# Performance work log

Measured on AMD Instinct MI355X. Metric: run time of the kernel, lower is better.

Reference implementation:

```python
import jax, jax.numpy as jnp
import numpy as np

N_NODES = 50000
N_EDGES = 800000
IN_C, HID_C, OUT_C = 128, 128, 64


def setup_inputs() -> dict:
    key = jax.random.key(0)
    ks = jax.random.split(key, 12)
    glorot = lambda k, shape: jax.random.normal(k, shape, dtype=jnp.float32) * (2.0 / (shape[0] + shape[-1])) ** 0.5
    return {
        "x": jax.random.normal(ks[0], (N_NODES, IN_C), dtype=jnp.float32),
        "edge_index": jax.random.randint(ks[1], (2, N_EDGES), 0, N_NODES, dtype=jnp.int64),
        "W_s1": glorot(ks[2], (IN_C, HID_C)), "b_s1": jnp.zeros((HID_C,), jnp.float32),
        "W_s2": glorot(ks[3], (HID_C, HID_C)), "b_s2": jnp.zeros((HID_C,), jnp.float32),
        "W_m1": glorot(ks[4], (IN_C, HID_C)), "b_m1": jnp.zeros((HID_C,), jnp.float32),
        "W_m21": glorot(ks[5], (IN_C, HID_C)), "b_m21": jnp.zeros((HID_C,), jnp.float32),
        "W_m22": glorot(ks[6], (HID_C, HID_C)), "b_m22": jnp.zeros((HID_C,), jnp.float32),
        "W_att": glorot(ks[7], (HID_C, 1)), "b_att": jnp.zeros((1,), jnp.float32),
        "W_fc": glorot(ks[8], (2 * HID_C, OUT_C)), "b_fc": jnp.zeros((OUT_C,), jnp.float32),
    }


def _gcn_conv(x, W, b, src, dst, n_nodes):
    """PyG GCNConv: add self-loops, symmetric deg^-1/2 norm, linear, scatter-add, bias."""
    xw = x @ W  # [N, H]
    loop = jnp.arange(n_nodes, dtype=src.dtype)
    s = jnp.concatenate([src, loop])
    d = jnp.concatenate([dst, loop])
    ones = jnp.ones(s.shape[0], dtype=x.dtype)
    deg = jax.ops.segment_sum(ones, d, num_segments=n_nodes)  # in-degree incl. self loop
    dinv = jnp.where(deg > 0, jax.lax.rsqrt(deg), 0.0)
    norm = dinv[s] * dinv[d]  # [E+N]
    msg = xw[s] * norm[:, None]
    return jax.ops.segment_sum(msg, d, num_segments=n_nodes) + b


def reference(x, edge_index, W_s1, b_s1, W_s2, b_s2, W_m1, b_m1, W_m21, b_m21,
              W_m22, b_m22, W_att, b_att, W_fc, b_fc):
    n = x.shape[0]
    src, dst = edge_index[0], edge_index[1]
    # structural branch: two GCN layers
    h_struct = jax.nn.relu(_gcn_conv(x, W_s1, b_s1, src, dst, n))
    h_struct = jax.nn.relu(_gcn_conv(h_struct, W_s2, b_s2, src, dst, n))
    # meta branches
    h1 = jax.nn.relu(_gcn_conv(x, W_m1, b_m1, src, dst, n))
    h2 = jax.nn.relu(_gcn_conv(x, W_m21, b_m21, src, dst, n))
    h2 = jax.nn.relu(_gcn_conv(h2, W_m22, b_m22, src, dst, n))
    # attention-weighted fusion over the 2 branches
    H = jnp.stack([h1, h2], axis=1)  # [N, 2, H]
    attn_scores = H @ W_att + b_att  # [N, 2, 1]
    attn_weights = jax.nn.softmax(attn_scores, axis=1)
    h_meta = jnp.sum(attn_weights * H, axis=1)  # [N, H]
    h_comb = jnp.concatenate([h_struct, h_meta], axis=1)  # [N, 2H]
    return h_comb @ W_fc + b_fc  # [N, OUT_C]
```

## Files before the change

kernel.cpp:

```cpp
#include <hip/hip_runtime.h>
#include <hip/hip_bf16.h>

#define N_NODES 50000
#define N_EDGES 800000

#define SCAN_BS 256
#define SCAN_NB ((N_NODES + SCAN_BS - 1) / SCAN_BS)

#define PREP_CVT_NB   6250
#define PREP_DEG_NB   3125
#define PREP_WCAT_NB  192
#define PREP_TP_NB    64
#define PREP_NB (PREP_CVT_NB + PREP_DEG_NB + PREP_WCAT_NB + 3 * PREP_TP_NB)

typedef __attribute__((ext_vector_type(8))) short bf16x8;
typedef __attribute__((ext_vector_type(4))) float f32x4;

__device__ __forceinline__ ushort f2bf(float f) {
    unsigned u = __float_as_uint(f);
    return (ushort)((u + 0x7fffu + ((u >> 16) & 1u)) >> 16);
}
__device__ __forceinline__ float bf2f(ushort u) {
    return __uint_as_float(((unsigned)u) << 16);
}

__global__ __launch_bounds__(256)
void prep_kernel(const float* __restrict__ x, uint2* __restrict__ xb4,
                 const int* __restrict__ edst, int* __restrict__ hist,
                 const float* __restrict__ Ws1, const float* __restrict__ Wm21,
                 const float* __restrict__ Wm1,
                 const float* __restrict__ bs1, const float* __restrict__ bm21,
                 const float* __restrict__ bm1,
                 ushort* __restrict__ Wcat_t, float* __restrict__ bcat,
                 const float* __restrict__ Ws2, ushort* __restrict__ Ws2t,
                 const float* __restrict__ Wm22, ushort* __restrict__ Wm22t,
                 const float* __restrict__ Wfc, ushort* __restrict__ Wfct,
                 int* __restrict__ row_ptr) {
    const int bid = blockIdx.x;
    const int t = threadIdx.x;
    if (bid < PREP_CVT_NB) {
        int i = bid * 256 + t;
        float4 v = *(const float4*)&x[(size_t)i * 4];
        uint2 o;
        o.x = (uint)f2bf(v.x) | ((uint)f2bf(v.y) << 16);
        o.y = (uint)f2bf(v.z) | ((uint)f2bf(v.w) << 16);
        xb4[i] = o;
    } else if (bid < PREP_CVT_NB + PREP_DEG_NB) {
        int e = (bid - PREP_CVT_NB) * 256 + t;
        atomicAdd(&hist[edst[e]], 1);
    } else if (bid < PREP_CVT_NB + PREP_DEG_NB + PREP_WCAT_NB) {
        int idx = (bid - PREP_CVT_NB - PREP_DEG_NB) * 256 + t;
        int c = idx >> 7, k = idx & 127;
        float v = (c < 128) ? Ws1[k * 128 + c]
                : (c < 256) ? Wm21[k * 128 + (c - 128)]
                            : Wm1[k * 128 + (c - 256)];
        Wcat_t[idx] = f2bf(v);
        if (idx < 384) {
            bcat[idx] = (idx < 128) ? bs1[idx] : (idx < 256) ? bm21[idx - 128] : bm1[idx - 256];
        }
        if (idx == 0) row_ptr[N_NODES] = N_EDGES;
    } else if (bid < PREP_CVT_NB + PREP_DEG_NB + PREP_WCAT_NB + PREP_TP_NB) {
        int idx = (bid - PREP_CVT_NB - PREP_DEG_NB - PREP_WCAT_NB) * 256 + t;
        int c = idx >> 7, k = idx & 127;
        Ws2t[idx] = f2bf(Ws2[(size_t)k * 128 + c]);
    } else if (bid < PREP_CVT_NB + PREP_DEG_NB + PREP_WCAT_NB + 2 * PREP_TP_NB) {
        int idx = (bid - PREP_CVT_NB - PREP_DEG_NB - PREP_WCAT_NB - PREP_TP_NB) * 256 + t;
        int c = idx >> 7, k = idx & 127;
        Wm22t[idx] = f2bf(Wm22[(size_t)k * 128 + c]);
    } else {
        int idx = (bid - PREP_CVT_NB - PREP_DEG_NB - PREP_WCAT_NB - 2 * PREP_TP_NB) * 256 + t;
        int c = idx >> 8, k = idx & 255;
        Wfct[idx] = f2bf(Wfc[(size_t)k * 64 + c]);
    }
}

__global__ __launch_bounds__(SCAN_BS)
void scan1_kernel(const int* __restrict__ hist, int* __restrict__ bsum,
                  float* __restrict__ dinv, int n) {
    __shared__ int s[SCAN_BS];
    int t = threadIdx.x;
    int i = blockIdx.x * SCAN_BS + t;
    int v = (i < n) ? hist[i] : 0;
    if (i < n) dinv[i] = rsqrtf((float)(v + 1));
    s[t] = v;
    __syncthreads();
#pragma unroll
    for (int off = SCAN_BS / 2; off > 0; off >>= 1) {
        if (t < off) s[t] += s[t + off];
        __syncthreads();
    }
    if (t == 0) bsum[blockIdx.x] = s[0];
}

__global__ __launch_bounds__(SCAN_BS)
void scan3_kernel(const int* __restrict__ hist, const int* __restrict__ bsum,
                  int* __restrict__ row_ptr, int* __restrict__ cursor, int n) {
    __shared__ int s[SCAN_BS];
    __shared__ int pre_s;
    int t = threadIdx.x;
    int b = blockIdx.x;
    int p = 0;
    for (int j = t; j < b; j += SCAN_BS) p += bsum[j];
    s[t] = p;
    __syncthreads();
#pragma unroll
    for (int off = SCAN_BS / 2; off > 0; off >>= 1) {
        if (t < off) s[t] += s[t + off];
        __syncthreads();
    }
    if (t == 0) pre_s = s[0];
    __syncthreads();
    const int pre = pre_s;
    __syncthreads();
    int i = b * SCAN_BS + t;
    int v = (i < n) ? hist[i] : 0;
    s[t] = v;
    __syncthreads();
#pragma unroll
    for (int off = 1; off < SCAN_BS; off <<= 1) {
        int tmp = (t >= off) ? s[t - off] : 0;
        __syncthreads();
        s[t] += tmp;
        __syncthreads();
    }
    if (i < n) {
        int ex = s[t] - v + pre;
        row_ptr[i] = ex;
        cursor[i]  = ex;
    }
}

__global__ void fill_kernel(const int* __restrict__ src, const int* __restrict__ dst, int E,
                            int* __restrict__ cursor, int2* __restrict__ edge_data,
                            const float* __restrict__ dinv) {
    int e = blockIdx.x * blockDim.x + threadIdx.x;
    if (e < E) {
        int d = dst[e];
        int s = src[e];
        int pos = atomicAdd(&cursor[d], 1);
        edge_data[pos] = make_int2(s, __float_as_int(dinv[s]));
    }
}

template<int C>
__global__ __launch_bounds__(256)
void agg_bf16(const ushort* __restrict__ X, int ldx,
              ushort* __restrict__ Y, int ldy,
              const int* __restrict__ row_ptr,
              const int2* __restrict__ edge_data,
              const float* __restrict__ dinv, int n) {
    constexpr int CG = C / 8;
    constexpr int SLOTS = 64 / CG;
    const int wid = blockIdx.x * (blockDim.x >> 6) + (threadIdx.x >> 6);
    if (wid >= n) return;
    const int lane = threadIdx.x & 63;
    const int cg = lane & (CG - 1);
    const int slot = lane / CG;

    const float di = dinv[wid];
    float acc[8] = {0.f, 0.f, 0.f, 0.f, 0.f, 0.f, 0.f, 0.f};

    auto fma_row = [&](uint4 v, float w) {
        acc[0] = fmaf(w, __uint_as_float(v.x << 16), acc[0]);
        acc[1] = fmaf(w, __uint_as_float(v.x & 0xffff0000u), acc[1]);
        acc[2] = fmaf(w, __uint_as_float(v.y << 16), acc[2]);
        acc[3] = fmaf(w, __uint_as_float(v.y & 0xffff0000u), acc[3]);
        acc[4] = fmaf(w, __uint_as_float(v.z << 16), acc[4]);
        acc[5] = fmaf(w, __uint_as_float(v.z & 0xffff0000u), acc[5]);
        acc[6] = fmaf(w, __uint_as_float(v.w << 16), acc[6]);
        acc[7] = fmaf(w, __uint_as_float(v.w & 0xffff0000u), acc[7]);
    };

    if (slot == 0) {
        uint4 v = *(const uint4*)&X[(size_t)wid * ldx + cg * 8];
        fma_row(v, di * di);
    }
    const int e0 = row_ptr[wid], e1 = row_ptr[wid + 1];
    int e = e0 + slot;
    for (; e + 3 * SLOTS < e1; e += 4 * SLOTS) {
        const int2 d0 = edge_data[e];
        const int2 d1 = edge_data[e + SLOTS];
        const int2 d2 = edge_data[e + 2 * SLOTS];
        const int2 d3 = edge_data[e + 3 * SLOTS];
        const uint4 v0 = *(const uint4*)&X[(size_t)d0.x * ldx + cg * 8];
        const uint4 v1 = *(const uint4*)&X[(size_t)d1.x * ldx + cg * 8];
        const uint4 v2 = *(const uint4*)&X[(size_t)d2.x * ldx + cg * 8];
        const uint4 v3 = *(const uint4*)&X[(size_t)d3.x * ldx + cg * 8];
        fma_row(v0, di * __int_as_float(d0.y));
        fma_row(v1, di * __int_as_float(d1.y));
        fma_row(v2, di * __int_as_float(d2.y));
        fma_row(v3, di * __int_as_float(d3.y));
    }
    for (; e < e1; e += SLOTS) {
        const int2 d0 = edge_data[e];
        const uint4 v0 = *(const uint4*)&X[(size_t)d0.x * ldx + cg * 8];
        fma_row(v0, di * __int_as_float(d0.y));
    }
#pragma unroll
    for (int j = 0; j < 8; ++j) {
        if (SLOTS == 4) acc[j] += __shfl_xor(acc[j], 16);
        if (SLOTS >= 2) acc[j] += __shfl_xor(acc[j], 32);
    }
    if (slot == 0) {
        uint4 o;
        o.x = (uint)f2bf(acc[0]) | ((uint)f2bf(acc[1]) << 16);
        o.y = (uint)f2bf(acc[2]) | ((uint)f2bf(acc[3]) << 16);
        o.z = (uint)f2bf(acc[4]) | ((uint)f2bf(acc[5]) << 16);
        o.w = (uint)f2bf(acc[6]) | ((uint)f2bf(acc[7]) << 16);
        *(uint4*)&Y[(size_t)wid * ldy + cg * 8] = o;
    }
}

__global__ __launch_bounds__(256)
void mfma_gemm_kernel(const ushort* __restrict__ A, int lda,
                      const ushort* __restrict__ Wt,
                      const float* __restrict__ bias,
                      ushort* __restrict__ Y, int ldy, int M) {
    __shared__ char Asmem[128 * 272];
    const int tid = threadIdx.x;
    const int lane = tid & 63;
    const int w = tid >> 6;
    const int rb = blockIdx.x * 128;
    const int cb = blockIdx.y * 128;

    {
        const int rowbase = tid >> 4;
        const int seg = tid & 15;
#pragma unroll
        for (int it = 0; it < 8; ++it) {
            int row = it * 16 + rowbase;
            uint4 v = make_uint4(0u, 0u, 0u, 0u);
            int r = rb + row;
            if (r < M) v = *(const uint4*)&A[(size_t)r * lda + seg * 8];
            *(uint4*)&Asmem[row * 272 + seg * 16] = v;
        }
    }
    __syncthreads();

    f32x4 acc[2][8];
#pragma unroll
    for (int i = 0; i < 2; ++i)
#pragma unroll
        for (int j = 0; j < 8; ++j) acc[i][j] = (f32x4){0.f, 0.f, 0.f, 0.f};

    const int arow0 = w * 32 + (lane & 15);
    const int kq = (lane >> 4) * 8;
    const int ccol = lane & 15;
#pragma unroll
    for (int ks = 0; ks < 4; ++ks) {
        const int k0 = ks * 32;
        const bf16x8 a0 = *(const bf16x8*)&Asmem[arow0 * 272 + (k0 + kq) * 2];
        const bf16x8 a1 = *(const bf16x8*)&Asmem[(arow0 + 16) * 272 + (k0 + kq) * 2];
#pragma unroll
        for (int ct = 0; ct < 8; ++ct) {
            const bf16x8 b = *(const bf16x8*)&Wt[(size_t)(cb + ct * 16 + ccol) * 128 + k0 + kq];
            acc[0][ct] = __builtin_amdgcn_mfma_f32_16x16x32_bf16(a0, b, acc[0][ct], 0, 0, 0);
            acc[1][ct] = __builtin_amdgcn_mfma_f32_16x16x32_bf16(a1, b, acc[1][ct], 0, 0, 0);
        }
    }

    const int rowq = (lane >> 4) * 4;
#pragma unroll
    for (int rt = 0; rt < 2; ++rt) {
#pragma unroll
        for (int ct = 0; ct < 8; ++ct) {
            const int col = cb + ct * 16 + ccol;
            const float bcol = bias[col];
#pragma unroll
            for (int r = 0; r < 4; ++r) {
                const int row = rb + w * 32 + rt * 16 + rowq + r;
                if (row >= M) continue;
                Y[(size_t)row * ldy + col] = f2bf(fmaxf(acc[rt][ct][r] + bcol, 0.f));
            }
        }
    }
}

__global__ __launch_bounds__(512, 4)
void gemm2fc_kernel(const ushort* __restrict__ bufB,
                    const ushort* __restrict__ Ws2t, const float* __restrict__ bs2,
                    const ushort* __restrict__ Wm22t, const float* __restrict__ bm22,
                    const ushort* __restrict__ cat1,
                    const float* __restrict__ Watt, const float* __restrict__ batt,
                    const ushort* __restrict__ Wfct, const float* __restrict__ bfc,
                    float* __restrict__ Y, int M) {
    __shared__ __align__(16) char smem[69632];
    const int tid = threadIdx.x;
    const int rb = blockIdx.x * 128;

    {
        const int seg = tid & 15;
        const int rowbase = tid >> 4;
#pragma unroll
        for (int it = 0; it < 8; ++it) {
            int idx = it * 32 + rowbase;
            int region = idx >> 7;
            int row = idx & 127;
            int r = rb + row;
            uint4 v = make_uint4(0u, 0u, 0u, 0u);
            if (r < M) v = *(const uint4*)&bufB[(size_t)r * 256 + region * 128 + seg * 8];
            *(uint4*)&smem[region * 34816 + row * 272 + seg * 16] = v;
        }
    }
    __syncthreads();

    const int w = tid >> 6;
    const int lane = tid & 63;
    const int branch = w >> 2;
    const int wl = w & 3;
    const char* Areg = smem + branch * 34816;
    const ushort* Wt = branch ? Wm22t : Ws2t;
    const float* bias = branch ? bm22 : bs2;

    f32x4 acc[2][8];
#pragma unroll
    for (int i = 0; i < 2; ++i)
#pragma unroll
        for (int j = 0; j < 8; ++j) acc[i][j] = (f32x4){0.f, 0.f, 0.f, 0.f};

    const int arow0 = wl * 32 + (lane & 15);
    const int kq = (lane >> 4) * 8;
    const int ccol = lane & 15;
#pragma unroll
    for (int ks = 0; ks < 4; ++ks) {
        const int k0 = ks * 32;
        const bf16x8 a0 = *(const bf16x8*)&Areg[arow0 * 272 + (k0 + kq) * 2];
        const bf16x8 a1 = *(const bf16x8*)&Areg[(arow0 + 16) * 272 + (k0 + kq) * 2];
#pragma unroll
        for (int ct = 0; ct < 8; ++ct) {
            const bf16x8 b = *(const bf16x8*)&Wt[(size_t)(ct * 16 + ccol) * 128 + k0 + kq];
            acc[0][ct] = __builtin_amdgcn_mfma_f32_16x16x32_bf16(a0, b, acc[0][ct], 0, 0, 0);
            acc[1][ct] = __builtin_amdgcn_mfma_f32_16x16x32_bf16(a1, b, acc[1][ct], 0, 0, 0);
        }
    }

#pragma unroll
    for (int rt = 0; rt < 2; ++rt)
#pragma unroll
        for (int ct = 0; ct < 8; ++ct) {
            const float bcol = bias[ct * 16 + ccol];
#pragma unroll
            for (int r = 0; r < 4; ++r)
                acc[rt][ct][r] = fmaxf(acc[rt][ct][r] + bcol, 0.f);
        }

    const int quad = lane >> 4;
    if (branch == 1) {
        float wv[8];
#pragma unroll
        for (int ct = 0; ct < 8; ++ct) wv[ct] = Watt[ct * 16 + ccol];
        const float ba = batt[0];
#pragma unroll
        for (int rt = 0; rt < 2; ++rt) {
#pragma unroll
            for (int r = 0; r < 4; ++r) {
                const int row0 = rb + wl * 32 + rt * 16 + quad * 4 + r;
                const int rowc = (row0 < M) ? row0 : (M - 1);
                const ushort* h1row = &cat1[(size_t)rowc * 384 + 256];
                float bp = 0.f, ap = 0.f;
#pragma unroll
                for (int ct = 0; ct < 8; ++ct) {
                    bp += acc[rt][ct][r] * wv[ct];
                    ap += bf2f(h1row[ct * 16 + ccol]) * wv[ct];
                }
#pragma unroll
                for (int off = 1; off < 16; off <<= 1) {
                    bp += __shfl_xor(bp, off);
                    ap += __shfl_xor(ap, off);
                }
                const float a = ap + ba, b = bp + ba;
                const float m = fmaxf(a, b);
                const float ea = __expf(a - m), eb = __expf(b - m);
                const float inv = 1.f / (ea + eb);
                const float wa = ea * inv, wb = eb * inv;
#pragma unroll
                for (int ct = 0; ct < 8; ++ct) {
                    const float h1 = bf2f(h1row[ct * 16 + ccol]);
                    acc[rt][ct][r] = fmaf(wa, h1, wb * acc[rt][ct][r]);
                }
            }
        }
    }
    __syncthreads();

#pragma unroll
    for (int rt = 0; rt < 2; ++rt) {
#pragma unroll
        for (int ct = 0; ct < 8; ++ct) {
            const int col = branch * 128 + ct * 16 + ccol;
#pragma unroll
            for (int r = 0; r < 4; ++r) {
                const int row = wl * 32 + rt * 16 + quad * 4 + r;
                *(ushort*)&smem[row * 528 + col * 2] = f2bf(acc[rt][ct][r]);
            }
        }
    }
    __syncthreads();

    f32x4 fcacc[4];
#pragma unroll
    for (int j = 0; j < 4; ++j) fcacc[j] = (f32x4){0.f, 0.f, 0.f, 0.f};
    const int frow = w * 16 + (lane & 15);
#pragma unroll
    for (int ks = 0; ks < 8; ++ks) {
        const int k0 = ks * 32;
        const bf16x8 a = *(const bf16x8*)&smem[frow * 528 + (k0 + kq) * 2];
#pragma unroll
        for (int ct = 0; ct < 4; ++ct) {
            const bf16x8 b = *(const bf16x8*)&Wfct[(size_t)(ct * 16 + ccol) * 256 + k0 + kq];
            fcacc[ct] = __builtin_amdgcn_mfma_f32_16x16x32_bf16(a, b, fcacc[ct], 0, 0, 0);
        }
    }
#pragma unroll
    for (int ct = 0; ct < 4; ++ct) {
        const int col = ct * 16 + ccol;
        const float bcol = bfc[col];
#pragma unroll
        for (int r = 0; r < 4; ++r) {
            const int row = rb + w * 16 + quad * 4 + r;
            if (row < M) Y[(size_t)row * 64 + col] = fcacc[ct][r] + bcol;
        }
    }
}

extern "C" void kernel_launch(void* const* d_in, const int* in_sizes, int n_in,
                              void* d_out, int out_size, void* d_ws, size_t ws_size,
                              hipStream_t stream) {
    const int N = N_NODES, E = N_EDGES;
    const float* x     = (const float*)d_in[0];
    const int*   ei    = (const int*)d_in[1];
    const int*   esrc  = ei;
    const int*   edst  = ei + E;
    const float* W_s1  = (const float*)d_in[2];
    const float* b_s1  = (const float*)d_in[3];
    const float* W_s2  = (const float*)d_in[4];
    const float* b_s2  = (const float*)d_in[5];
    const float* W_m1  = (const float*)d_in[6];
    const float* b_m1  = (const float*)d_in[7];
    const float* W_m21 = (const float*)d_in[8];
    const float* b_m21 = (const float*)d_in[9];
    const float* W_m22 = (const float*)d_in[10];
    const float* b_m22 = (const float*)d_in[11];
    const float* W_att = (const float*)d_in[12];
    const float* b_att = (const float*)d_in[13];
    const float* W_fc  = (const float*)d_in[14];
    const float* b_fc  = (const float*)d_in[15];
    float* out = (float*)d_out;

    char* base = (char*)d_ws;
    size_t off = 0;
    auto take = [&](size_t nbytes) -> void* {
        void* p = base + off;
        off += (nbytes + 255) & ~(size_t)255;
        return p;
    };
    int*    hist      = (int*)take((size_t)N * 4);
    int*    cursor    = (int*)take((size_t)N * 4);
    int*    row_ptr   = (int*)take((size_t)(N + 1) * 4);
    int*    bsum      = (int*)take((size_t)SCAN_NB * 4);
    int2*   edge_data = (int2*)take((size_t)E * 8);
    float*  dinv      = (float*)take((size_t)N * 4);
    ushort* xb        = (ushort*)take((size_t)N * 128 * 2);
    ushort* agg_x     = (ushort*)take((size_t)N * 128 * 2);
    ushort* cat1      = (ushort*)take((size_t)N * 384 * 2);
    ushort* bufB      = (ushort*)take((size_t)N * 256 * 2);
    ushort* Wcat_t    = (ushort*)take((size_t)384 * 128 * 2);
    ushort* Ws2_t     = (ushort*)take((size_t)128 * 128 * 2);
    ushort* Wm22_t    = (ushort*)take((size_t)128 * 128 * 2);
    ushort* Wfc_t     = (ushort*)take((size_t)64 * 256 * 2);
    float*  bcat      = (float*)take((size_t)384 * 4);

    hipMemsetAsync(hist, 0, (size_t)N * 4, stream);
    prep_kernel<<<PREP_NB, 256, 0, stream>>>(x, (uint2*)xb, edst, hist,
                                             W_s1, W_m21, W_m1, b_s1, b_m21, b_m1,
                                             Wcat_t, bcat, W_s2, Ws2_t, W_m22, Wm22_t,
                                             W_fc, Wfc_t, row_ptr);
    scan1_kernel<<<SCAN_NB, SCAN_BS, 0, stream>>>(hist, bsum, dinv, N);
    scan3_kernel<<<SCAN_NB, SCAN_BS, 0, stream>>>(hist, bsum, row_ptr, cursor, N);
    fill_kernel<<<(E + 255) / 256, 256, 0, stream>>>(esrc, edst, E, cursor, edge_data, dinv);

    agg_bf16<128><<<(N + 3) / 4, 256, 0, stream>>>(xb, 128, agg_x, 128, row_ptr, edge_data, dinv, N);
    dim3 gm384((N + 127) / 128, 3);
    mfma_gemm_kernel<<<gm384, 256, 0, stream>>>(agg_x, 128, Wcat_t, bcat, cat1, 384, N);
    agg_bf16<256><<<(N + 3) / 4, 256, 0, stream>>>(cat1, 384, bufB, 256, row_ptr, edge_data, dinv, N);
    gemm2fc_kernel<<<(N + 127) / 128, 512, 0, stream>>>(bufB, Ws2_t, b_s2, Wm22_t, b_m22,
                                                        cat1, W_att, b_att, Wfc_t, b_fc, out, N);
}
```

Measured before the change: 375.7 us.

## Slice feature matrices into 32-channel planes for cache-friendly gather aggregation

Node features are stored as separate 32-column slices, each contiguous across nodes, and the aggregation kernel gives each block one slice. The goal is a smaller gather working set per slice, so repeated neighbor rows stay in L2/MALL and fewer 64-byte lines are fetched per edge. In exchange, edge lists and row pointers are re-read once per slice, and the GEMM epilogue now writes scattered slice-layout output with per-column branching. The h1 branch is split into its own buffer.

```diff
diff --git a/kernel.cpp b/kernel.cpp
--- a/kernel.cpp
+++ b/kernel.cpp
@@ -25,7 +25,7 @@
 }
 
 __global__ __launch_bounds__(256)
-void prep_kernel(const float* __restrict__ x, uint2* __restrict__ xb4,
+void prep_kernel(const float* __restrict__ x, uint2* __restrict__ xbs4,
                  const int* __restrict__ edst, int* __restrict__ hist,
                  const float* __restrict__ Ws1, const float* __restrict__ Wm21,
                  const float* __restrict__ Wm1,
@@ -44,7 +44,11 @@
         uint2 o;
         o.x = (uint)f2bf(v.x) | ((uint)f2bf(v.y) << 16);
         o.y = (uint)f2bf(v.z) | ((uint)f2bf(v.w) << 16);
-        xb4[i] = o;
+        int node = i >> 5;
+        int g = i & 31;
+        int slice = g >> 3;
+        int wi = g & 7;
+        xbs4[((size_t)slice * N_NODES + node) * 8 + wi] = o;
     } else if (bid < PREP_CVT_NB + PREP_DEG_NB) {
         int e = (bid - PREP_CVT_NB) * 256 + t;
         atomicAdd(&hist[edst[e]], 1);
@@ -142,72 +146,73 @@
     }
 }
 
-template<int C>
+template<int NSLICES>
 __global__ __launch_bounds__(256)
-void agg_bf16(const ushort* __restrict__ X, int ldx,
-              ushort* __restrict__ Y, int ldy,
-              const int* __restrict__ row_ptr,
-              const int2* __restrict__ edge_data,
-              const float* __restrict__ dinv, int n) {
-    constexpr int CG = C / 8;
-    constexpr int SLOTS = 64 / CG;
-    const int wid = blockIdx.x * (blockDim.x >> 6) + (threadIdx.x >> 6);
-    if (wid >= n) return;
-    const int lane = threadIdx.x & 63;
-    const int cg = lane & (CG - 1);
-    const int slot = lane / CG;
-
-    const float di = dinv[wid];
-    float acc[8] = {0.f, 0.f, 0.f, 0.f, 0.f, 0.f, 0.f, 0.f};
-
-    auto fma_row = [&](uint4 v, float w) {
-        acc[0] = fmaf(w, __uint_as_float(v.x << 16), acc[0]);
-        acc[1] = fmaf(w, __uint_as_float(v.x & 0xffff0000u), acc[1]);
-        acc[2] = fmaf(w, __uint_as_float(v.y << 16), acc[2]);
-        acc[3] = fmaf(w, __uint_as_float(v.y & 0xffff0000u), acc[3]);
-        acc[4] = fmaf(w, __uint_as_float(v.z << 16), acc[4]);
-        acc[5] = fmaf(w, __uint_as_float(v.z & 0xffff0000u), acc[5]);
-        acc[6] = fmaf(w, __uint_as_float(v.w << 16), acc[6]);
-        acc[7] = fmaf(w, __uint_as_float(v.w & 0xffff0000u), acc[7]);
-    };
-
-    if (slot == 0) {
-        uint4 v = *(const uint4*)&X[(size_t)wid * ldx + cg * 8];
-        fma_row(v, di * di);
-    }
-    const int e0 = row_ptr[wid], e1 = row_ptr[wid + 1];
-    int e = e0 + slot;
-    for (; e + 3 * SLOTS < e1; e += 4 * SLOTS) {
-        const int2 d0 = edge_data[e];
-        const int2 d1 = edge_data[e + SLOTS];
-        const int2 d2 = edge_data[e + 2 * SLOTS];
-        const int2 d3 = edge_data[e + 3 * SLOTS];
-        const uint4 v0 = *(const uint4*)&X[(size_t)d0.x * ldx + cg * 8];
-        const uint4 v1 = *(const uint4*)&X[(size_t)d1.x * ldx + cg * 8];
-        const uint4 v2 = *(const uint4*)&X[(size_t)d2.x * ldx + cg * 8];
-        const uint4 v3 = *(const uint4*)&X[(size_t)d3.x * ldx + cg * 8];
-        fma_row(v0, di * __int_as_float(d0.y));
-        fma_row(v1, di * __int_as_float(d1.y));
-        fma_row(v2, di * __int_as_float(d2.y));
-        fma_row(v3, di * __int_as_float(d3.y));
-    }
-    for (; e < e1; e += SLOTS) {
-        const int2 d0 = edge_data[e];
-        const uint4 v0 = *(const uint4*)&X[(size_t)d0.x * ldx + cg * 8];
-        fma_row(v0, di * __int_as_float(d0.y));
-    }
-#pragma unroll
-    for (int j = 0; j < 8; ++j) {
-        if (SLOTS == 4) acc[j] += __shfl_xor(acc[j], 16);
-        if (SLOTS >= 2) acc[j] += __shfl_xor(acc[j], 32);
-    }
-    if (slot == 0) {
-        uint4 o;
-        o.x = (uint)f2bf(acc[0]) | ((uint)f2bf(acc[1]) << 16);
-        o.y = (uint)f2bf(acc[2]) | ((uint)f2bf(acc[3]) << 16);
-        o.z = (uint)f2bf(acc[4]) | ((uint)f2bf(acc[5]) << 16);
-        o.w = (uint)f2bf(acc[6]) | ((uint)f2bf(acc[7]) << 16);
-        *(uint4*)&Y[(size_t)wid * ldy + cg * 8] = o;
+void agg_sliced(const ushort* __restrict__ Xs,
+                ushort* __restrict__ Y, int ldy,
+                const int* __restrict__ row_ptr,
+                const int2* __restrict__ edge_data,
+                const float* __restrict__ dinv, int n) {
+    const int slice = blockIdx.x % NSLICES;
+    const int grp   = blockIdx.x / NSLICES;
+    const int wave  = threadIdx.x >> 6;
+    const int lane  = threadIdx.x & 63;
+    const int chunk = lane & 3;
+    const int slot  = lane >> 2;
+    const ushort* X = Xs + (size_t)slice * n * 32;
+
+#pragma unroll 1
+    for (int nd = 0; nd < 4; ++nd) {
+        const int node = grp * 16 + wave * 4 + nd;
+        if (node >= n) break;
+        const float di = dinv[node];
+        float acc[8] = {0.f, 0.f, 0.f, 0.f, 0.f, 0.f, 0.f, 0.f};
+
+        auto fma_row = [&](uint4 v, float w) {
+            acc[0] = fmaf(w, __uint_as_float(v.x << 16), acc[0]);
+            acc[1] = fmaf(w, __uint_as_float(v.x & 0xffff0000u), acc[1]);
+            acc[2] = fmaf(w, __uint_as_float(v.y << 16), acc[2]);
+            acc[3] = fmaf(w, __uint_as_float(v.y & 0xffff0000u), acc[3]);
+            acc[4] = fmaf(w, __uint_as_float(v.z << 16), acc[4]);
+            acc[5] = fmaf(w, __uint_as_float(v.z & 0xffff0000u), acc[5]);
+            acc[6] = fmaf(w, __uint_as_float(v.w << 16), acc[6]);
+            acc[7] = fmaf(w, __uint_as_float(v.w & 0xffff0000u), acc[7]);
+        };
+
+        if (slot == 0) {
+            uint4 v = *(const uint4*)&X[(size_t)node * 32 + chunk * 8];
+            fma_row(v, di * di);
+        }
+        const int e0 = row_ptr[node], e1 = row_ptr[node + 1];
+        int e = e0 + slot;
+        for (; e + 16 < e1; e += 32) {
+            const int2 d0 = edge_data[e];
+            const int2 d1 = edge_data[e + 16];
+            const uint4 v0 = *(const uint4*)&X[(size_t)d0.x * 32 + chunk * 8];
+            const uint4 v1 = *(const uint4*)&X[(size_t)d1.x * 32 + chunk * 8];
+            fma_row(v0, di * __int_as_float(d0.y));
+            fma_row(v1, di * __int_as_float(d1.y));
+        }
+        if (e < e1) {
+            const int2 d0 = edge_data[e];
+            const uint4 v0 = *(const uint4*)&X[(size_t)d0.x * 32 + chunk * 8];
+            fma_row(v0, di * __int_as_float(d0.y));
+        }
+#pragma unroll
+        for (int j = 0; j < 8; ++j) {
+            acc[j] += __shfl_xor(acc[j], 4);
+            acc[j] += __shfl_xor(acc[j], 8);
+            acc[j] += __shfl_xor(acc[j], 16);
+            acc[j] += __shfl_xor(acc[j], 32);
+        }
+        if (slot == 0) {
+            uint4 o;
+            o.x = (uint)f2bf(acc[0]) | ((uint)f2bf(acc[1]) << 16);
+            o.y = (uint)f2bf(acc[2]) | ((uint)f2bf(acc[3]) << 16);
+            o.z = (uint)f2bf(acc[4]) | ((uint)f2bf(acc[5]) << 16);
+            o.w = (uint)f2bf(acc[6]) | ((uint)f2bf(acc[7]) << 16);
+            *(uint4*)&Y[(size_t)node * ldy + slice * 32 + chunk * 8] = o;
+        }
     }
 }
 
@@ -215,7 +220,7 @@
 void mfma_gemm_kernel(const ushort* __restrict__ A, int lda,
                       const ushort* __restrict__ Wt,
                       const float* __restrict__ bias,
-                      ushort* __restrict__ Y, int ldy, int M) {
+                      ushort* __restrict__ catA, ushort* __restrict__ h1, int M) {
     __shared__ char Asmem[128 * 272];
     const int tid = threadIdx.x;
     const int lane = tid & 63;
@@ -265,12 +270,16 @@
 #pragma unroll
         for (int ct = 0; ct < 8; ++ct) {
             const int col = cb + ct * 16 + ccol;
-            const float bcol = bias[col];
 #pragma unroll
             for (int r = 0; r < 4; ++r) {
                 const int row = rb + w * 32 + rt * 16 + rowq + r;
                 if (row >= M) continue;
-                Y[(size_t)row * ldy + col] = f2bf(fmaxf(acc[rt][ct][r] + bcol, 0.f));
+                float v = fmaxf(acc[rt][ct][r] + bias[col], 0.f);
+                ushort bv = f2bf(v);
+                if (col < 256)
+                    catA[((size_t)(col >> 5) * N_NODES + row) * 32 + (col & 31)] = bv;
+                else
+                    h1[(size_t)row * 128 + (col - 256)] = bv;
             }
         }
     }
@@ -280,7 +289,7 @@
 void gemm2fc_kernel(const ushort* __restrict__ bufB,
                     const ushort* __restrict__ Ws2t, const float* __restrict__ bs2,
                     const ushort* __restrict__ Wm22t, const float* __restrict__ bm22,
-                    const ushort* __restrict__ cat1,
+                    const ushort* __restrict__ h1buf,
                     const float* __restrict__ Watt, const float* __restrict__ batt,
                     const ushort* __restrict__ Wfct, const float* __restrict__ bfc,
                     float* __restrict__ Y, int M) {
@@ -356,7 +365,7 @@
             for (int r = 0; r < 4; ++r) {
                 const int row0 = rb + wl * 32 + rt * 16 + quad * 4 + r;
                 const int rowc = (row0 < M) ? row0 : (M - 1);
-                const ushort* h1row = &cat1[(size_t)rowc * 384 + 256];
+                const ushort* h1row = &h1buf[(size_t)rowc * 128];
                 float bp = 0.f, ap = 0.f;
 #pragma unroll
                 for (int ct = 0; ct < 8; ++ct) {
@@ -460,9 +469,10 @@
     int*    bsum      = (int*)take((size_t)SCAN_NB * 4);
     int2*   edge_data = (int2*)take((size_t)E * 8);
     float*  dinv      = (float*)take((size_t)N * 4);
-    ushort* xb        = (ushort*)take((size_t)N * 128 * 2);
+    ushort* xbs       = (ushort*)take((size_t)N * 128 * 2);
     ushort* agg_x     = (ushort*)take((size_t)N * 128 * 2);
-    ushort* cat1      = (ushort*)take((size_t)N * 384 * 2);
+    ushort* catA      = (ushort*)take((size_t)N * 256 * 2);
+    ushort* h1buf     = (ushort*)take((size_t)N * 128 * 2);
     ushort* bufB      = (ushort*)take((size_t)N * 256 * 2);
     ushort* Wcat_t    = (ushort*)take((size_t)384 * 128 * 2);
     ushort* Ws2_t     = (ushort*)take((size_t)128 * 128 * 2);
@@ -471,7 +481,7 @@
     float*  bcat      = (float*)take((size_t)384 * 4);
 
     hipMemsetAsync(hist, 0, (size_t)N * 4, stream);
-    prep_kernel<<<PREP_NB, 256, 0, stream>>>(x, (uint2*)xb, edst, hist,
+    prep_kernel<<<PREP_NB, 256, 0, stream>>>(x, (uint2*)xbs, edst, hist,
                                              W_s1, W_m21, W_m1, b_s1, b_m21, b_m1,
                                              Wcat_t, bcat, W_s2, Ws2_t, W_m22, Wm22_t,
                                              W_fc, Wfc_t, row_ptr);
@@ -479,10 +489,11 @@
     scan3_kernel<<<SCAN_NB, SCAN_BS, 0, stream>>>(hist, bsum, row_ptr, cursor, N);
     fill_kernel<<<(E + 255) / 256, 256, 0, stream>>>(esrc, edst, E, cursor, edge_data, dinv);
 
-    agg_bf16<128><<<(N + 3) / 4, 256, 0, stream>>>(xb, 128, agg_x, 128, row_ptr, edge_data, dinv, N);
+    const int NGRP = (N + 15) / 16;
+    agg_sliced<4><<<NGRP * 4, 256, 0, stream>>>(xbs, agg_x, 128, row_ptr, edge_data, dinv, N);
     dim3 gm384((N + 127) / 128, 3);
-    mfma_gemm_kernel<<<gm384, 256, 0, stream>>>(agg_x, 128, Wcat_t, bcat, cat1, 384, N);
-    agg_bf16<256><<<(N + 3) / 4, 256, 0, stream>>>(cat1, 384, bufB, 256, row_ptr, edge_data, dinv, N);
+    mfma_gemm_kernel<<<gm384, 256, 0, stream>>>(agg_x, 128, Wcat_t, bcat, catA, h1buf, N);
+    agg_sliced<8><<<NGRP * 8, 256, 0, stream>>>(catA, bufB, 256, row_ptr, edge_data, dinv, N);
     gemm2fc_kernel<<<(N + 127) / 128, 512, 0, stream>>>(bufB, Ws2_t, b_s2, Wm22_t, b_m22,
-                                                        cat1, W_att, b_att, Wfc_t, b_fc, out, N);
-}
+                                                        h1buf, W_att, b_att, Wfc_t, b_fc, out, N);
+}
```

New measurement: 496.1 us. 1.32x slower.

## Fuse first-layer neighbor aggregation into the 384-wide MFMA GEMM kernel

Applied to the files above, without the earlier changes.

Merges the bf16 aggregation of x and the first-layer GEMM into one kernel. Each wave aggregates 16 nodes into shared memory, then runs MFMA against all 384 output columns. This removes the agg_x intermediate's global write and re-read plus one launch. In exchange each wave processes its 16 nodes one after another (4 edge slots per node instead of wave-per-node), the block count drops, and each wave holds 24 accumulator tiles, so occupancy and latency hiding may suffer.

```diff
diff --git a/kernel.cpp b/kernel.cpp
--- a/kernel.cpp
+++ b/kernel.cpp
@@ -212,66 +212,107 @@
 }
 
 __global__ __launch_bounds__(256)
-void mfma_gemm_kernel(const ushort* __restrict__ A, int lda,
+void agg_gemm1_kernel(const ushort* __restrict__ xb,
+                      const int* __restrict__ row_ptr,
+                      const int2* __restrict__ edge_data,
+                      const float* __restrict__ dinv,
                       const ushort* __restrict__ Wt,
                       const float* __restrict__ bias,
-                      ushort* __restrict__ Y, int ldy, int M) {
-    __shared__ char Asmem[128 * 272];
+                      ushort* __restrict__ cat1, int n) {
+    __shared__ __align__(16) char smem[64 * 272];
     const int tid = threadIdx.x;
+    const int w = tid >> 6;
     const int lane = tid & 63;
-    const int w = tid >> 6;
-    const int rb = blockIdx.x * 128;
-    const int cb = blockIdx.y * 128;
-
-    {
-        const int rowbase = tid >> 4;
-        const int seg = tid & 15;
-#pragma unroll
-        for (int it = 0; it < 8; ++it) {
-            int row = it * 16 + rowbase;
-            uint4 v = make_uint4(0u, 0u, 0u, 0u);
-            int r = rb + row;
-            if (r < M) v = *(const uint4*)&A[(size_t)r * lda + seg * 8];
-            *(uint4*)&Asmem[row * 272 + seg * 16] = v;
-        }
-    }
-    __syncthreads();
-
-    f32x4 acc[2][8];
-#pragma unroll
-    for (int i = 0; i < 2; ++i)
-#pragma unroll
-        for (int j = 0; j < 8; ++j) acc[i][j] = (f32x4){0.f, 0.f, 0.f, 0.f};
-
-    const int arow0 = w * 32 + (lane & 15);
+    const int rb = blockIdx.x * 64;
+    const int row0 = w * 16;
+    char* myrows = smem + row0 * 272;
+
+    const int cg = lane & 15;
+    const int slot = lane >> 4;
+#pragma unroll 1
+    for (int nd = 0; nd < 16; ++nd) {
+        const int node = rb + row0 + nd;
+        float acc[8] = {0.f, 0.f, 0.f, 0.f, 0.f, 0.f, 0.f, 0.f};
+        auto fma_row = [&](uint4 v, float wgt) {
+            acc[0] = fmaf(wgt, __uint_as_float(v.x << 16), acc[0]);
+            acc[1] = fmaf(wgt, __uint_as_float(v.x & 0xffff0000u), acc[1]);
+            acc[2] = fmaf(wgt, __uint_as_float(v.y << 16), acc[2]);
+            acc[3] = fmaf(wgt, __uint_as_float(v.y & 0xffff0000u), acc[3]);
+            acc[4] = fmaf(wgt, __uint_as_float(v.z << 16), acc[4]);
+            acc[5] = fmaf(wgt, __uint_as_float(v.z & 0xffff0000u), acc[5]);
+            acc[6] = fmaf(wgt, __uint_as_float(v.w << 16), acc[6]);
+            acc[7] = fmaf(wgt, __uint_as_float(v.w & 0xffff0000u), acc[7]);
+        };
+        if (node < n) {
+            const float di = dinv[node];
+            if (slot == 0) {
+                uint4 v = *(const uint4*)&xb[(size_t)node * 128 + cg * 8];
+                fma_row(v, di * di);
+            }
+            const int e0 = row_ptr[node], e1 = row_ptr[node + 1];
+            int e = e0 + slot;
+            for (; e + 12 < e1; e += 16) {
+                const int2 d0 = edge_data[e];
+                const int2 d1 = edge_data[e + 4];
+                const int2 d2 = edge_data[e + 8];
+                const int2 d3 = edge_data[e + 12];
+                const uint4 v0 = *(const uint4*)&xb[(size_t)d0.x * 128 + cg * 8];
+                const uint4 v1 = *(const uint4*)&xb[(size_t)d1.x * 128 + cg * 8];
+                const uint4 v2 = *(const uint4*)&xb[(size_t)d2.x * 128 + cg * 8];
+                const uint4 v3 = *(const uint4*)&xb[(size_t)d3.x * 128 + cg * 8];
+                fma_row(v0, di * __int_as_float(d0.y));
+                fma_row(v1, di * __int_as_float(d1.y));
+                fma_row(v2, di * __int_as_float(d2.y));
+                fma_row(v3, di * __int_as_float(d3.y));
+            }
+            for (; e < e1; e += 4) {
+                const int2 d0 = edge_data[e];
+                const uint4 v0 = *(const uint4*)&xb[(size_t)d0.x * 128 + cg * 8];
+                fma_row(v0, di * __int_as_float(d0.y));
+            }
+        }
+#pragma unroll
+        for (int j = 0; j < 8; ++j) {
+            acc[j] += __shfl_xor(acc[j], 16);
+            acc[j] += __shfl_xor(acc[j], 32);
+        }
+        if (slot == 0) {
+            uint4 o;
+            o.x = (uint)f2bf(acc[0]) | ((uint)f2bf(acc[1]) << 16);
+            o.y = (uint)f2bf(acc[2]) | ((uint)f2bf(acc[3]) << 16);
+            o.z = (uint)f2bf(acc[4]) | ((uint)f2bf(acc[5]) << 16);
+            o.w = (uint)f2bf(acc[6]) | ((uint)f2bf(acc[7]) << 16);
+            *(uint4*)&myrows[nd * 272 + cg * 16] = o;
+        }
+    }
+
+    f32x4 acc2[24];
+#pragma unroll
+    for (int j = 0; j < 24; ++j) acc2[j] = (f32x4){0.f, 0.f, 0.f, 0.f};
+    const int arow = lane & 15;
     const int kq = (lane >> 4) * 8;
     const int ccol = lane & 15;
 #pragma unroll
     for (int ks = 0; ks < 4; ++ks) {
         const int k0 = ks * 32;
-        const bf16x8 a0 = *(const bf16x8*)&Asmem[arow0 * 272 + (k0 + kq) * 2];
-        const bf16x8 a1 = *(const bf16x8*)&Asmem[(arow0 + 16) * 272 + (k0 + kq) * 2];
-#pragma unroll
-        for (int ct = 0; ct < 8; ++ct) {
-            const bf16x8 b = *(const bf16x8*)&Wt[(size_t)(cb + ct * 16 + ccol) * 128 + k0 + kq];
-            acc[0][ct] = __builtin_amdgcn_mfma_f32_16x16x32_bf16(a0, b, acc[0][ct], 0, 0, 0);
-            acc[1][ct] = __builtin_amdgcn_mfma_f32_16x16x32_bf16(a1, b, acc[1][ct], 0, 0, 0);
+        const bf16x8 a = *(const bf16x8*)&myrows[arow * 272 + (k0 + kq) * 2];
+#pragma unroll
+        for (int ct = 0; ct < 24; ++ct) {
+            const bf16x8 b = *(const bf16x8*)&Wt[(size_t)(ct * 16 + ccol) * 128 + k0 + kq];
+            acc2[ct] = __builtin_amdgcn_mfma_f32_16x16x32_bf16(a, b, acc2[ct], 0, 0, 0);
         }
     }
 
     const int rowq = (lane >> 4) * 4;
 #pragma unroll
-    for (int rt = 0; rt < 2; ++rt) {
-#pragma unroll
-        for (int ct = 0; ct < 8; ++ct) {
-            const int col = cb + ct * 16 + ccol;
-            const float bcol = bias[col];
-#pragma unroll
-            for (int r = 0; r < 4; ++r) {
-                const int row = rb + w * 32 + rt * 16 + rowq + r;
-                if (row >= M) continue;
-                Y[(size_t)row * ldy + col] = f2bf(fmaxf(acc[rt][ct][r] + bcol, 0.f));
-            }
+    for (int ct = 0; ct < 24; ++ct) {
+        const int col = ct * 16 + ccol;
+        const float bcol = bias[col];
+#pragma unroll
+        for (int r = 0; r < 4; ++r) {
+            const int row = rb + row0 + rowq + r;
+            if (row < n)
+                cat1[(size_t)row * 384 + col] = f2bf(fmaxf(acc2[ct][r] + bcol, 0.f));
         }
     }
 }
@@ -461,7 +502,6 @@
     int2*   edge_data = (int2*)take((size_t)E * 8);
     float*  dinv      = (float*)take((size_t)N * 4);
     ushort* xb        = (ushort*)take((size_t)N * 128 * 2);
-    ushort* agg_x     = (ushort*)take((size_t)N * 128 * 2);
     ushort* cat1      = (ushort*)take((size_t)N * 384 * 2);
     ushort* bufB      = (ushort*)take((size_t)N * 256 * 2);
     ushort* Wcat_t    = (ushort*)take((size_t)384 * 128 * 2);
@@ -479,9 +519,8 @@
     scan3_kernel<<<SCAN_NB, SCAN_BS, 0, stream>>>(hist, bsum, row_ptr, cursor, N);
     fill_kernel<<<(E + 255) / 256, 256, 0, stream>>>(esrc, edst, E, cursor, edge_data, dinv);
 
-    agg_bf16<128><<<(N + 3) / 4, 256, 0, stream>>>(xb, 128, agg_x, 128, row_ptr, edge_data, dinv, N);
-    dim3 gm384((N + 127) / 128, 3);
-    mfma_gemm_kernel<<<gm384, 256, 0, stream>>>(agg_x, 128, Wcat_t, bcat, cat1, 384, N);
+    agg_gemm1_kernel<<<(N + 63) / 64, 256, 0, stream>>>(xb, row_ptr, edge_data, dinv,
+                                                        Wcat_t, bcat, cat1, N);
     agg_bf16<256><<<(N + 3) / 4, 256, 0, stream>>>(cat1, 384, bufB, 256, row_ptr, edge_data, dinv, N);
     gemm2fc_kernel<<<(N + 127) / 128, 512, 0, stream>>>(bufB, Ws2_t, b_s2, Wm22_t, b_m22,
                                                         cat1, W_att, b_att, Wfc_t, b_fc, out, N);
```

Result: slower. 443.9 us (+18.2%).

## Record edge rank during degree histogram and split cat1 into contiguous buffers

Applied to the files above, without the earlier changes.

The degree-count atomic now returns each edge's slot, which is stored so the CSR fill computes positions as row_ptr plus rank instead of issuing a second round of atomics. The cursor array and its initialisation are removed. The first GEMM's 384-wide output is also split into a dense 256-wide buffer for the next aggregation and a separate 128-wide h1 buffer, so the 256-channel gather reads rows with a tighter stride. This costs an extra E-sized int array write and read, and adds a per-element branch in the GEMM epilogue.

```diff
diff --git a/kernel.cpp b/kernel.cpp
--- a/kernel.cpp
+++ b/kernel.cpp
@@ -27,6 +27,7 @@
 __global__ __launch_bounds__(256)
 void prep_kernel(const float* __restrict__ x, uint2* __restrict__ xb4,
                  const int* __restrict__ edst, int* __restrict__ hist,
+                 int* __restrict__ rank,
                  const float* __restrict__ Ws1, const float* __restrict__ Wm21,
                  const float* __restrict__ Wm1,
                  const float* __restrict__ bs1, const float* __restrict__ bm21,
@@ -47,7 +48,7 @@
         xb4[i] = o;
     } else if (bid < PREP_CVT_NB + PREP_DEG_NB) {
         int e = (bid - PREP_CVT_NB) * 256 + t;
-        atomicAdd(&hist[edst[e]], 1);
+        rank[e] = atomicAdd(&hist[edst[e]], 1);
     } else if (bid < PREP_CVT_NB + PREP_DEG_NB + PREP_WCAT_NB) {
         int idx = (bid - PREP_CVT_NB - PREP_DEG_NB) * 256 + t;
         int c = idx >> 7, k = idx & 127;
@@ -94,7 +95,7 @@
 
 __global__ __launch_bounds__(SCAN_BS)
 void scan3_kernel(const int* __restrict__ hist, const int* __restrict__ bsum,
-                  int* __restrict__ row_ptr, int* __restrict__ cursor, int n) {
+                  int* __restrict__ row_ptr, int n) {
     __shared__ int s[SCAN_BS];
     __shared__ int pre_s;
     int t = threadIdx.x;
@@ -123,21 +124,18 @@
         s[t] += tmp;
         __syncthreads();
     }
-    if (i < n) {
-        int ex = s[t] - v + pre;
-        row_ptr[i] = ex;
-        cursor[i]  = ex;
-    }
+    if (i < n) row_ptr[i] = s[t] - v + pre;
 }
 
 __global__ void fill_kernel(const int* __restrict__ src, const int* __restrict__ dst, int E,
-                            int* __restrict__ cursor, int2* __restrict__ edge_data,
+                            const int* __restrict__ row_ptr, const int* __restrict__ rank,
+                            int2* __restrict__ edge_data,
                             const float* __restrict__ dinv) {
     int e = blockIdx.x * blockDim.x + threadIdx.x;
     if (e < E) {
         int d = dst[e];
         int s = src[e];
-        int pos = atomicAdd(&cursor[d], 1);
+        int pos = row_ptr[d] + rank[e];
         edge_data[pos] = make_int2(s, __float_as_int(dinv[s]));
     }
 }
@@ -215,7 +213,7 @@
 void mfma_gemm_kernel(const ushort* __restrict__ A, int lda,
                       const ushort* __restrict__ Wt,
                       const float* __restrict__ bias,
-                      ushort* __restrict__ Y, int ldy, int M) {
+                      ushort* __restrict__ catA, ushort* __restrict__ h1, int M) {
     __shared__ char Asmem[128 * 272];
     const int tid = threadIdx.x;
     const int lane = tid & 63;
@@ -265,12 +263,14 @@
 #pragma unroll
         for (int ct = 0; ct < 8; ++ct) {
             const int col = cb + ct * 16 + ccol;
-            const float bcol = bias[col];
 #pragma unroll
             for (int r = 0; r < 4; ++r) {
                 const int row = rb + w * 32 + rt * 16 + rowq + r;
                 if (row >= M) continue;
-                Y[(size_t)row * ldy + col] = f2bf(fmaxf(acc[rt][ct][r] + bcol, 0.f));
+                float v = fmaxf(acc[rt][ct][r] + bias[col], 0.f);
+                ushort bv = f2bf(v);
+                if (col < 256) catA[(size_t)row * 256 + col] = bv;
+                else           h1[(size_t)row * 128 + (col - 256)] = bv;
             }
         }
     }
@@ -280,7 +280,7 @@
 void gemm2fc_kernel(const ushort* __restrict__ bufB,
                     const ushort* __restrict__ Ws2t, const float* __restrict__ bs2,
                     const ushort* __restrict__ Wm22t, const float* __restrict__ bm22,
-                    const ushort* __restrict__ cat1,
+                    const ushort* __restrict__ h1buf,
                     const float* __restrict__ Watt, const float* __restrict__ batt,
                     const ushort* __restrict__ Wfct, const float* __restrict__ bfc,
                     float* __restrict__ Y, int M) {
@@ -356,7 +356,7 @@
             for (int r = 0; r < 4; ++r) {
                 const int row0 = rb + wl * 32 + rt * 16 + quad * 4 + r;
                 const int rowc = (row0 < M) ? row0 : (M - 1);
-                const ushort* h1row = &cat1[(size_t)rowc * 384 + 256];
+                const ushort* h1row = &h1buf[(size_t)rowc * 128];
                 float bp = 0.f, ap = 0.f;
 #pragma unroll
                 for (int ct = 0; ct < 8; ++ct) {
@@ -455,14 +455,15 @@
         return p;
     };
     int*    hist      = (int*)take((size_t)N * 4);
-    int*    cursor    = (int*)take((size_t)N * 4);
     int*    row_ptr   = (int*)take((size_t)(N + 1) * 4);
     int*    bsum      = (int*)take((size_t)SCAN_NB * 4);
+    int*    rank      = (int*)take((size_t)E * 4);
     int2*   edge_data = (int2*)take((size_t)E * 8);
     float*  dinv      = (float*)take((size_t)N * 4);
     ushort* xb        = (ushort*)take((size_t)N * 128 * 2);
     ushort* agg_x     = (ushort*)take((size_t)N * 128 * 2);
-    ushort* cat1      = (ushort*)take((size_t)N * 384 * 2);
+    ushort* catA      = (ushort*)take((size_t)N * 256 * 2);
+    ushort* h1buf     = (ushort*)take((size_t)N * 128 * 2);
     ushort* bufB      = (ushort*)take((size_t)N * 256 * 2);
     ushort* Wcat_t    = (ushort*)take((size_t)384 * 128 * 2);
     ushort* Ws2_t     = (ushort*)take((size_t)128 * 128 * 2);
@@ -471,18 +472,19 @@
     float*  bcat      = (float*)take((size_t)384 * 4);
 
     hipMemsetAsync(hist, 0, (size_t)N * 4, stream);
-    prep_kernel<<<PREP_NB, 256, 0, stream>>>(x, (uint2*)xb, edst, hist,
+    prep_kernel<<<PREP_NB, 256, 0, stream>>>(x, (uint2*)xb, edst, hist, rank,
                                              W_s1, W_m21, W_m1, b_s1, b_m21, b_m1,
                                              Wcat_t, bcat, W_s2, Ws2_t, W_m22, Wm22_t,
                                              W_fc, Wfc_t, row_ptr);
     scan1_kernel<<<SCAN_NB, SCAN_BS, 0, stream>>>(hist, bsum, dinv, N);
-    scan3_kernel<<<SCAN_NB, SCAN_BS, 0, stream>>>(hist, bsum, row_ptr, cursor, N);
-    fill_kernel<<<(E + 255) / 256, 256, 0, stream>>>(esrc, edst, E, cursor, edge_data, dinv);
+    scan3_kernel<<<SCAN_NB, SCAN_BS, 0, stream>>>(hist, bsum, row_ptr, N);
+    fill_kernel<<<(E + 255) / 256, 256, 0, stream>>>(esrc, edst, E, row_ptr, rank,
+                                                     edge_data, dinv);
 
     agg_bf16<128><<<(N + 3) / 4, 256, 0, stream>>>(xb, 128, agg_x, 128, row_ptr, edge_data, dinv, N);
     dim3 gm384((N + 127) / 128, 3);
-    mfma_gemm_kernel<<<gm384, 256, 0, stream>>>(agg_x, 128, Wcat_t, bcat, cat1, 384, N);
-    agg_bf16<256><<<(N + 3) / 4, 256, 0, stream>>>(cat1, 384, bufB, 256, row_ptr, edge_data, dinv, N);
+    mfma_gemm_kernel<<<gm384, 256, 0, stream>>>(agg_x, 128, Wcat_t, bcat, catA, h1buf, N);
+    agg_bf16<256><<<(N + 3) / 4, 256, 0, stream>>>(catA, 256, bufB, 256, row_ptr, edge_data, dinv, N);
     gemm2fc_kernel<<<(N + 127) / 128, 512, 0, stream>>>(bufB, Ws2_t, b_s2, Wm22_t, b_m22,
-                                                        cat1, W_att, b_att, Wfc_t, b_fc, out, N);
-}
+                                                        h1buf, W_att, b_att, Wfc_t, b_fc, out, N);
+}
```

Measured after the change: 345.8 us. 8.0% less time.
